# Optimization experiments

Measured on AMD Instinct MI355X. Metric: run time of the kernel, lower is better.

Reference implementation:

```python
import jax, jax.numpy as jnp
import numpy as np

IN, OUT, RANK, ALPHA, NSUB = 4096, 4096, 16, 32, 4
SCALING = ALPHA / RANK


def setup_inputs() -> dict:
    key = jax.random.key(0)
    ks = jax.random.split(key, 8)
    B, S = 4, 2048
    return {
        "x": jax.random.normal(ks[0], (B, S, IN), dtype=jnp.float32),
        "base_W": jax.random.normal(ks[1], (OUT, IN), dtype=jnp.float32) * 0.02,
        "base_b": jax.random.normal(ks[2], (OUT,), dtype=jnp.float32) * 0.02,
        "base_A": jax.random.normal(ks[3], (RANK, IN), dtype=jnp.float32) * 0.02,
        "base_B": jax.random.normal(ks[4], (OUT, RANK), dtype=jnp.float32) * 0.02,
        "sub_wgate": jax.random.normal(ks[5], (NSUB, IN), dtype=jnp.float32) * 0.02,
        "sub_A": jax.random.normal(ks[6], (NSUB, RANK, IN), dtype=jnp.float32) * 0.02,
        "sub_B": jax.random.normal(ks[7], (NSUB, OUT, RANK), dtype=jnp.float32) * 0.02,
    }


def reference(x, base_W, base_b, base_A, base_B, sub_wgate, sub_A, sub_B):
    # base linear: [B,S,IN] @ [IN,OUT] + bias
    out = jnp.einsum("bsd,od->bso", x, base_W) + base_b
    # base LoRA: x @ A^T @ B^T
    out = out + SCALING * jnp.einsum("bsr,or->bso", jnp.einsum("bsd,rd->bsr", x, base_A), base_B)
    # stacked ReLU-gated sub-adapters, batched over adapter dim j
    gates = jax.nn.relu(jnp.einsum("bsd,jd->bsj", x, sub_wgate))        # [B,S,J]
    mid = jnp.einsum("bsd,jrd->bsjr", x, sub_A)                           # [B,S,J,R] (small)
    # gate * (mid @ B^T) == (gate*mid) @ B^T since gate is per-token scalar
    gated_mid = mid * gates[..., None]
    out = out + SCALING * jnp.einsum("bsjr,jor->bso", gated_mid, sub_B)
    return out
```

## Files before the change

### kernel.cpp

```cpp
#include <hip/hip_runtime.h>
#include <hip/hip_bf16.h>
#include <stdint.h>

#define DIN   4096
#define DOUT  4096
#define RANK  16
#define NSUB  4
#define MTOT  8192
#define LDK   4160
#define KTAIL 64
#define NV    80

typedef __attribute__((ext_vector_type(8)))  short    short8;
typedef __attribute__((ext_vector_type(4)))  float    floatx4;
typedef __attribute__((ext_vector_type(8)))  unsigned short ushort8;
typedef __attribute__((ext_vector_type(4)))  unsigned short ushort4v;

static __device__ __forceinline__ unsigned short f2bf(float f) {
    unsigned int u = __float_as_uint(f);
    unsigned int r = (u + 0x7FFFu + ((u >> 16) & 1u)) >> 16;
    return (unsigned short)r;
}

static __device__ __forceinline__ void async_copy16(const unsigned short* g, unsigned short* l) {
    __builtin_amdgcn_global_load_lds(
        (const __attribute__((address_space(1))) unsigned int*)g,
        (__attribute__((address_space(3))) unsigned int*)l,
        16, 0, 0);
}

__global__ __launch_bounds__(256) void build_v_kernel(
    const float* __restrict__ sub_wgate,
    const float* __restrict__ sub_A,
    unsigned short* __restrict__ Vc)
{
    const int t = threadIdx.x;
    const int row = blockIdx.x;
    const float* src = (row < 64) ? (sub_A + (size_t)row * DIN)
                     : (row < 68) ? (sub_wgate + (size_t)(row - 64) * DIN)
                     : nullptr;
#pragma unroll
    for (int i = 0; i < 4; ++i) {
        int c4 = t + 256 * i;
        ushort4v v;
        if (src) {
            float4 a = ((const float4*)src)[c4];
            v[0] = f2bf(a.x); v[1] = f2bf(a.y); v[2] = f2bf(a.z); v[3] = f2bf(a.w);
        } else {
            v[0] = v[1] = v[2] = v[3] = 0;
        }
        *(ushort4v*)(Vc + (size_t)row * DIN + c4 * 4) = v;
    }
}

#define BXK 256
#define LDA 264
__global__ __launch_bounds__(256) void build_x_kernel(
    const float* __restrict__ x,
    const unsigned short* __restrict__ Vc,
    unsigned short* __restrict__ Xc)
{
    __shared__ char smem[(16 + NV) * LDA * 2];
    unsigned short* As = (unsigned short*)smem;
    unsigned short* Bs = As + 16 * LDA;
    float* Pp = (float*)smem;

    const int t  = threadIdx.x;
    const int l  = t & 63;
    const int w  = t >> 6;
    const int m0 = blockIdx.x * 16;
    const int lane16 = l & 15;
    const int kq     = (l >> 4) * 8;

    floatx4 acc[5] = {};

    for (int cc = 0; cc < DIN; cc += BXK) {
#pragma unroll
        for (int i = 0; i < 2; ++i) {
            int u8 = t + 256 * i;
            int tr = u8 >> 5;
            int c8 = u8 & 31;
            const float4* src = (const float4*)(x + (size_t)(m0 + tr) * DIN + cc + c8 * 8);
            float4 a = src[0], b = src[1];
            ushort8 v;
            v[0] = f2bf(a.x); v[1] = f2bf(a.y); v[2] = f2bf(a.z); v[3] = f2bf(a.w);
            v[4] = f2bf(b.x); v[5] = f2bf(b.y); v[6] = f2bf(b.z); v[7] = f2bf(b.w);
            *(ushort8*)&As[tr * LDA + c8 * 8] = v;
            *(ushort8*)(Xc + (size_t)(m0 + tr) * LDK + cc + c8 * 8) = v;
        }
#pragma unroll
        for (int i = 0; i < 10; ++i) {
            int idx = t + 256 * i;
            int vr  = idx >> 5;
            int c8  = idx & 31;
            ushort8 v = *(const ushort8*)(Vc + (size_t)vr * DIN + cc + c8 * 8);
            *(ushort8*)&Bs[vr * LDA + c8 * 8] = v;
        }
        __syncthreads();

#pragma unroll
        for (int s = 0; s < 2; ++s) {
            int ks = w * 2 + s;
            short8 af = *(const short8*)&As[lane16 * LDA + ks * 32 + kq];
#pragma unroll
            for (int n = 0; n < 5; ++n) {
                short8 bf = *(const short8*)&Bs[(n * 16 + lane16) * LDA + ks * 32 + kq];
                acc[n] = __builtin_amdgcn_mfma_f32_16x16x32_bf16(af, bf, acc[n], 0, 0, 0);
            }
        }
        __syncthreads();
    }

#pragma unroll
    for (int n = 0; n < 5; ++n)
#pragma unroll
        for (int r = 0; r < 4; ++r)
            Pp[(w * 16 + (l >> 4) * 4 + r) * NV + n * 16 + lane16] = acc[n][r];
    __syncthreads();

#pragma unroll
    for (int i = 0; i < 4; ++i) {
        int v  = t + 256 * i;
        int tr = v >> 6;
        int c  = v & 63;
        int j  = c >> 4;
        float ps = 0.f, gs = 0.f;
#pragma unroll
        for (int q = 0; q < 4; ++q) {
            ps += Pp[(q * 16 + tr) * NV + c];
            gs += Pp[(q * 16 + tr) * NV + 64 + j];
        }
        Xc[(size_t)(m0 + tr) * LDK + DIN + c] = f2bf(2.0f * fmaxf(gs, 0.f) * ps);
    }
}

__global__ __launch_bounds__(256) void build_w_kernel(
    const float* __restrict__ W,
    const float* __restrict__ base_A,
    const float* __restrict__ base_B,
    const float* __restrict__ sub_B,
    unsigned short* __restrict__ Wc)
{
    __shared__ float bBs[8 * RANK];

    const int t  = threadIdx.x;
    const int o0 = (blockIdx.x >> 2) * 8;
    const int cc = (blockIdx.x & 3) * 1024;
    const int q  = (cc >> 2) + t;

    if (t < 128) bBs[t] = 2.0f * base_B[(size_t)o0 * RANK + t];
    __syncthreads();

    float4 acc[8];
#pragma unroll
    for (int o = 0; o < 8; ++o)
        acc[o] = ((const float4*)(W + (size_t)(o0 + o) * DIN))[q];

#pragma unroll
    for (int r = 0; r < RANK; ++r) {
        float4 a = ((const float4*)(base_A + (size_t)r * DIN))[q];
#pragma unroll
        for (int o = 0; o < 8; ++o) {
            float s = bBs[o * RANK + r];
            acc[o].x += s * a.x; acc[o].y += s * a.y;
            acc[o].z += s * a.z; acc[o].w += s * a.w;
        }
    }

#pragma unroll
    for (int o = 0; o < 8; ++o) {
        ushort4v v;
        v[0] = f2bf(acc[o].x); v[1] = f2bf(acc[o].y);
        v[2] = f2bf(acc[o].z); v[3] = f2bf(acc[o].w);
        *(ushort4v*)(Wc + (size_t)(o0 + o) * LDK + q * 4) = v;
    }

    if ((blockIdx.x & 3) == 0) {
#pragma unroll
        for (int i = 0; i < 2; ++i) {
            int v = t + 256 * i;
            int o = v >> 6;
            int c = v & 63;
            int j = c >> 4;
            int r = c & 15;
            float s = sub_B[((size_t)j * DOUT + (o0 + o)) * RANK + r];
            Wc[(size_t)(o0 + o) * LDK + DIN + c] = f2bf(s);
        }
    }
}

__global__ __launch_bounds__(256) void gemm_kernel(
    const unsigned short* __restrict__ Xc,
    const unsigned short* __restrict__ Wc,
    const float* __restrict__ bias,
    float* __restrict__ out)
{
    __shared__ unsigned short As[128 * 32];
    __shared__ unsigned short Bs[128 * 32];

    const int t  = threadIdx.x;
    const int l  = t & 63;
    const int w  = t >> 6;
    const int wm = w >> 1;
    const int wn = w & 1;
    const int m0 = blockIdx.y * 128;
    const int n0 = blockIdx.x * 128;

    floatx4 acc[4][4] = {};

    const int srow = t >> 2;
    const int skc  = (t & 3) * 8;
    const unsigned short* gA = Xc + (size_t)(m0 + srow) * LDK + skc;
    const unsigned short* gB = Wc + (size_t)(n0 + srow) * LDK + skc;
    unsigned short* lA = &As[t * 8];
    unsigned short* lB = &Bs[t * 8];

    const int kq   = (l >> 4) * 8;
    const int lane16 = l & 15;

    for (int kk = 0; kk < LDK; kk += 32) {
        async_copy16(gA + kk, lA);
        async_copy16(gA + kk + (size_t)64 * LDK, lA + 64 * 32);
        async_copy16(gB + kk, lB);
        async_copy16(gB + kk + (size_t)64 * LDK, lB + 64 * 32);
        __syncthreads();

        short8 af[4], bf[4];
#pragma unroll
        for (int i = 0; i < 4; ++i) {
            af[i] = *(const short8*)&As[(wm * 64 + i * 16 + lane16) * 32 + kq];
            bf[i] = *(const short8*)&Bs[(wn * 64 + i * 16 + lane16) * 32 + kq];
        }
#pragma unroll
        for (int i = 0; i < 4; ++i)
#pragma unroll
            for (int j = 0; j < 4; ++j)
                acc[i][j] = __builtin_amdgcn_mfma_f32_16x16x32_bf16(af[i], bf[j], acc[i][j], 0, 0, 0);
        __syncthreads();
    }

    const int row_l = (l >> 4) * 4;
#pragma unroll
    for (int j = 0; j < 4; ++j) {
        int gcol = n0 + wn * 64 + j * 16 + lane16;
        float bv = bias[gcol];
#pragma unroll
        for (int i = 0; i < 4; ++i) {
            int grow = m0 + wm * 64 + i * 16 + row_l;
            size_t base = (size_t)grow * DOUT + gcol;
            out[base]            = acc[i][j][0] + bv;
            out[base + DOUT]     = acc[i][j][1] + bv;
            out[base + 2 * DOUT] = acc[i][j][2] + bv;
            out[base + 3 * DOUT] = acc[i][j][3] + bv;
        }
    }
}

extern "C" void kernel_launch(void* const* d_in, const int* in_sizes, int n_in,
                              void* d_out, int out_size, void* d_ws, size_t ws_size,
                              hipStream_t stream) {
    const float* x         = (const float*)d_in[0];
    const float* base_W    = (const float*)d_in[1];
    const float* base_b    = (const float*)d_in[2];
    const float* base_A    = (const float*)d_in[3];
    const float* base_B    = (const float*)d_in[4];
    const float* sub_wgate = (const float*)d_in[5];
    const float* sub_A     = (const float*)d_in[6];
    const float* sub_B     = (const float*)d_in[7];
    float* out = (float*)d_out;

    unsigned short* Xc = (unsigned short*)d_ws;
    unsigned short* Wc = Xc + (size_t)MTOT * LDK;
    unsigned short* Vc = Wc + (size_t)DOUT * LDK;

    build_v_kernel<<<NV, 256, 0, stream>>>(sub_wgate, sub_A, Vc);
    build_x_kernel<<<MTOT / 16, 256, 0, stream>>>(x, Vc, Xc);
    build_w_kernel<<<(DOUT / 8) * 4, 256, 0, stream>>>(base_W, base_A, base_B, sub_B, Wc);
    gemm_kernel<<<dim3(DOUT / 128, MTOT / 128), 256, 0, stream>>>(Xc, Wc, base_b, out);
}
```

Baseline: 626.2 us.

## Swizzle LDS layouts, deepen GEMM K-step to 64, async-load gate weights

The main GEMM now stages 128x64 K-slabs per iteration instead of 128x32, using an XOR-swizzled LDS layout so MFMA fragment reads avoid bank conflicts. This halves the number of barriers per K pass. The gate/adapter weight matrix Vc is repacked into 256-column chunks so build_x can fetch it with async global-to-LDS copies into a swizzled layout, replacing register round-trips. The risks are more LDS per block, which could lower occupancy, and unchanged single buffering with no load/compute overlap.

```diff
diff --git a/kernel.cpp b/kernel.cpp
--- a/kernel.cpp
+++ b/kernel.cpp
@@ -49,18 +49,19 @@
         } else {
             v[0] = v[1] = v[2] = v[3] = 0;
         }
-        *(ushort4v*)(Vc + (size_t)row * DIN + c4 * 4) = v;
-    }
-}
-
-#define BXK 256
-#define LDA 264
+        int chunk = c4 >> 6;
+        int cin   = (c4 * 4) & 255;
+        *(ushort4v*)(Vc + ((size_t)chunk * NV + row) * 256 + cin) = v;
+    }
+}
+
+#define LDA 272
 __global__ __launch_bounds__(256) void build_x_kernel(
     const float* __restrict__ x,
     const unsigned short* __restrict__ Vc,
     unsigned short* __restrict__ Xc)
 {
-    __shared__ char smem[(16 + NV) * LDA * 2];
+    __shared__ char smem[16 * LDA * 2 + NV * 256 * 2];
     unsigned short* As = (unsigned short*)smem;
     unsigned short* Bs = As + 16 * LDA;
     float* Pp = (float*)smem;
@@ -70,11 +71,20 @@
     const int w  = t >> 6;
     const int m0 = blockIdx.x * 16;
     const int lane16 = l & 15;
-    const int kq     = (l >> 4) * 8;
+    const int q      = l >> 4;
+    const int kq     = q * 8;
 
     floatx4 acc[5] = {};
 
-    for (int cc = 0; cc < DIN; cc += BXK) {
+    for (int cc = 0; cc < DIN; cc += 256) {
+        const unsigned short* slab = Vc + (size_t)(cc >> 8) * (NV * 256);
+#pragma unroll
+        for (int j = 0; j < 10; ++j) {
+            int sb  = w * 10 + j;
+            int row = sb * 2 + (l >> 5);
+            const unsigned short* g = slab + row * 256 + (((l & 31) ^ (row & 7)) * 8);
+            async_copy16(g, Bs + sb * 512 + l * 8);
+        }
 #pragma unroll
         for (int i = 0; i < 2; ++i) {
             int u8 = t + 256 * i;
@@ -88,23 +98,16 @@
             *(ushort8*)&As[tr * LDA + c8 * 8] = v;
             *(ushort8*)(Xc + (size_t)(m0 + tr) * LDK + cc + c8 * 8) = v;
         }
-#pragma unroll
-        for (int i = 0; i < 10; ++i) {
-            int idx = t + 256 * i;
-            int vr  = idx >> 5;
-            int c8  = idx & 31;
-            ushort8 v = *(const ushort8*)(Vc + (size_t)vr * DIN + cc + c8 * 8);
-            *(ushort8*)&Bs[vr * LDA + c8 * 8] = v;
-        }
         __syncthreads();
 
 #pragma unroll
         for (int s = 0; s < 2; ++s) {
             int ks = w * 2 + s;
             short8 af = *(const short8*)&As[lane16 * LDA + ks * 32 + kq];
+            int C = ks * 4 + q;
 #pragma unroll
             for (int n = 0; n < 5; ++n) {
-                short8 bf = *(const short8*)&Bs[(n * 16 + lane16) * LDA + ks * 32 + kq];
+                short8 bf = *(const short8*)&Bs[(n * 16 + lane16) * 256 + ((C ^ (lane16 & 7)) * 8)];
                 acc[n] = __builtin_amdgcn_mfma_f32_16x16x32_bf16(af, bf, acc[n], 0, 0, 0);
             }
         }
@@ -115,7 +118,7 @@
     for (int n = 0; n < 5; ++n)
 #pragma unroll
         for (int r = 0; r < 4; ++r)
-            Pp[(w * 16 + (l >> 4) * 4 + r) * NV + n * 16 + lane16] = acc[n][r];
+            Pp[(w * 16 + q * 4 + r) * NV + n * 16 + lane16] = acc[n][r];
     __syncthreads();
 
 #pragma unroll
@@ -126,9 +129,9 @@
         int j  = c >> 4;
         float ps = 0.f, gs = 0.f;
 #pragma unroll
-        for (int q = 0; q < 4; ++q) {
-            ps += Pp[(q * 16 + tr) * NV + c];
-            gs += Pp[(q * 16 + tr) * NV + 64 + j];
+        for (int qq = 0; qq < 4; ++qq) {
+            ps += Pp[(qq * 16 + tr) * NV + c];
+            gs += Pp[(qq * 16 + tr) * NV + 64 + j];
         }
         Xc[(size_t)(m0 + tr) * LDK + DIN + c] = f2bf(2.0f * fmaxf(gs, 0.f) * ps);
     }
@@ -195,51 +198,66 @@
     const float* __restrict__ bias,
     float* __restrict__ out)
 {
-    __shared__ unsigned short As[128 * 32];
-    __shared__ unsigned short Bs[128 * 32];
+    __shared__ unsigned short smem[16384];
+    unsigned short* As = smem;
+    unsigned short* Bs = smem + 8192;
 
     const int t  = threadIdx.x;
     const int l  = t & 63;
-    const int w  = t >> 6;
-    const int wm = w >> 1;
-    const int wn = w & 1;
+    const int wm = (t >> 6) >> 1;
+    const int wn = (t >> 6) & 1;
     const int m0 = blockIdx.y * 128;
     const int n0 = blockIdx.x * 128;
 
     floatx4 acc[4][4] = {};
 
-    const int srow = t >> 2;
-    const int skc  = (t & 3) * 8;
-    const unsigned short* gA = Xc + (size_t)(m0 + srow) * LDK + skc;
-    const unsigned short* gB = Wc + (size_t)(n0 + srow) * LDK + skc;
-    unsigned short* lA = &As[t * 8];
-    unsigned short* lB = &Bs[t * 8];
-
-    const int kq   = (l >> 4) * 8;
+    const int row_i = t >> 3;
+    const int slot  = t & 7;
+    const int fch   = slot ^ (row_i & 7);
+    const unsigned short* gA[4];
+    const unsigned short* gB[4];
+    unsigned short *lA[4], *lB[4];
+#pragma unroll
+    for (int i = 0; i < 4; ++i) {
+        int row = i * 32 + row_i;
+        gA[i] = Xc + (size_t)(m0 + row) * LDK + fch * 8;
+        gB[i] = Wc + (size_t)(n0 + row) * LDK + fch * 8;
+        lA[i] = As + i * 2048 + t * 8;
+        lB[i] = Bs + i * 2048 + t * 8;
+    }
+
+    const int q      = l >> 4;
     const int lane16 = l & 15;
-
-    for (int kk = 0; kk < LDK; kk += 32) {
-        async_copy16(gA + kk, lA);
-        async_copy16(gA + kk + (size_t)64 * LDK, lA + 64 * 32);
-        async_copy16(gB + kk, lB);
-        async_copy16(gB + kk + (size_t)64 * LDK, lB + 64 * 32);
-        __syncthreads();
-
-        short8 af[4], bf[4];
+    const int sw     = lane16 & 7;
+
+    for (int kk = 0; kk < LDK; kk += 64) {
 #pragma unroll
         for (int i = 0; i < 4; ++i) {
-            af[i] = *(const short8*)&As[(wm * 64 + i * 16 + lane16) * 32 + kq];
-            bf[i] = *(const short8*)&Bs[(wn * 64 + i * 16 + lane16) * 32 + kq];
-        }
-#pragma unroll
-        for (int i = 0; i < 4; ++i)
-#pragma unroll
-            for (int j = 0; j < 4; ++j)
-                acc[i][j] = __builtin_amdgcn_mfma_f32_16x16x32_bf16(af[i], bf[j], acc[i][j], 0, 0, 0);
-        __syncthreads();
-    }
-
-    const int row_l = (l >> 4) * 4;
+            async_copy16(gA[i] + kk, lA[i]);
+            async_copy16(gB[i] + kk, lB[i]);
+        }
+        __syncthreads();
+
+#pragma unroll
+        for (int ks2 = 0; ks2 < 2; ++ks2) {
+            int C = ks2 * 4 + q;
+            int Cs = (C ^ sw) * 8;
+            short8 af[4], bf[4];
+#pragma unroll
+            for (int i = 0; i < 4; ++i) {
+                af[i] = *(const short8*)&As[(wm * 64 + i * 16 + lane16) * 64 + Cs];
+                bf[i] = *(const short8*)&Bs[(wn * 64 + i * 16 + lane16) * 64 + Cs];
+            }
+#pragma unroll
+            for (int i = 0; i < 4; ++i)
+#pragma unroll
+                for (int j = 0; j < 4; ++j)
+                    acc[i][j] = __builtin_amdgcn_mfma_f32_16x16x32_bf16(af[i], bf[j], acc[i][j], 0, 0, 0);
+        }
+        __syncthreads();
+    }
+
+    const int row_l = q * 4;
 #pragma unroll
     for (int j = 0; j < 4; ++j) {
         int gcol = n0 + wn * 64 + j * 16 + lane16;
```

After: 638.7 us. About the same (+2.0%).
